# Kernel optimization log

Hardware: AMD Instinct MI355X
Metric: run time of the kernel (lower is better)

The kernel has to match this reference:

```python
import jax, jax.numpy as jnp
import numpy as np

P = 2          # SamplesLoss p=2
BLUR = 0.05    # eps_final = BLUR**P = 0.0025
SCALING = 0.8  # annealing factor per iteration (on the blur scale)


def _cost(x, y):
    # geomloss cost for p=2: |x - y|^2 / 2, shape (N, M)
    x2 = jnp.sum(x * x, axis=-1)
    y2 = jnp.sum(y * y, axis=-1)
    return 0.5 * (x2[:, None] + y2[None, :] - 2.0 * (x @ y.T))


def _softmin(eps, C, h):
    # -eps * log sum_j exp(h_j - C_ij / eps); h already contains log-weights
    return -eps * jax.nn.logsumexp(h[None, :] - C / eps, axis=1)


def _eps_schedule(x, y):
    # geomloss scaling_parameters / epsilon_schedule with diameter from bounding box
    xn, yn = np.asarray(x), np.asarray(y)
    mins = np.minimum(xn.min(0), yn.min(0))
    maxs = np.maximum(xn.max(0), yn.max(0))
    diameter = float(np.linalg.norm(maxs - mins))
    eps_list = ([diameter ** P]
                + [float(np.exp(e)) for e in np.arange(P * np.log(diameter), P * np.log(BLUR), P * np.log(SCALING))]
                + [BLUR ** P])
    return eps_list


def _sinkhorn_divergence(x, y, eps_list):
    # Debiased Sinkhorn divergence S_eps(x, y), geomloss sinkhorn_tensorized
    N, M = x.shape[0], y.shape[0]
    sg = jax.lax.stop_gradient
    C_xy, C_yx = _cost(x, y), _cost(y, x)
    C_xx, C_yy = _cost(x, sg(x)), _cost(y, sg(y))  # geomloss detaches 2nd arg
    # The annealing loop runs with autograd disabled in geomloss:
    Cxy_, Cyx_, Cxx_, Cyy_ = sg(C_xy), sg(C_yx), sg(C_xx), sg(C_yy)
    a_log = jnp.full((N,), -np.log(N), dtype=x.dtype)  # log uniform weights
    b_log = jnp.full((M,), -np.log(M), dtype=y.dtype)
    e0 = eps_list[0]
    f_aa = _softmin(e0, Cxx_, a_log)
    g_bb = _softmin(e0, Cyy_, b_log)
    g_ab = _softmin(e0, Cyx_, a_log)
    f_ba = _softmin(e0, Cxy_, b_log)
    for eps in eps_list:  # fixed schedule, not a data-dim loop
        ft_ba = _softmin(eps, Cxy_, b_log + g_ab / eps)
        gt_ab = _softmin(eps, Cyx_, a_log + f_ba / eps)
        ft_aa = _softmin(eps, Cxx_, a_log + f_aa / eps)
        gt_bb = _softmin(eps, Cyy_, b_log + g_bb / eps)
        f_ba, g_ab = 0.5 * (f_ba + ft_ba), 0.5 * (g_ab + gt_ab)
        f_aa, g_bb = 0.5 * (f_aa + ft_aa), 0.5 * (g_bb + gt_bb)
    # Final extrapolation step (the only one geomloss differentiates through):
    eps = eps_list[-1]
    f_ba, g_ab = (_softmin(eps, C_xy, sg(b_log + g_ab / eps)),
                  _softmin(eps, C_yx, sg(a_log + f_ba / eps)))
    f_aa = _softmin(eps, C_xx, sg(a_log + f_aa / eps))
    g_bb = _softmin(eps, C_yy, sg(b_log + g_bb / eps))
    # scal with uniform weights == mean
    return jnp.mean(f_ba - f_aa) + jnp.mean(g_ab - g_bb)


def setup_inputs() -> dict:
    key = jax.random.key(0)
    kx, kt = jax.random.split(key)
    x = jax.random.normal(kx, (4096, 64), dtype=jnp.float32)
    target = jax.random.normal(kt, (4096, 64), dtype=jnp.float32)
    return {"x": x, "target": target}


def reference(x, target):
    eps_list = _eps_schedule(x, target)  # concrete schedule from data diameter
    return _sinkhorn_divergence(x, target, eps_list)
```

## Files before the change

### kernel.cpp

```cpp
#include <hip/hip_runtime.h>
#include <math.h>

#define NPTS 4096
#define DIM  64
#define MAX_ITERS 37

#define ALOG (-8.317766166719343f)
#define L2E  (1.4426950408889634f)
#define LN2  (0.6931471805599453f)

#define SEA 8388608.0f
#define SEB 1064872507.0f

#if __has_builtin(__builtin_amdgcn_exp2f)
#define EXP2F(x) __builtin_amdgcn_exp2f(x)
#else
#define EXP2F(x) exp2f(x)
#endif
#if __has_builtin(__builtin_amdgcn_logf)
#define LOG2F(x) __builtin_amdgcn_logf(x)
#else
#define LOG2F(x) log2f(x)
#endif

typedef _Float16 f16x8 __attribute__((ext_vector_type(8)));
typedef float    f32x4 __attribute__((ext_vector_type(4)));

__device__ __forceinline__ float aload(const float* p) {
    return __hip_atomic_load(p, __ATOMIC_RELAXED, __HIP_MEMORY_SCOPE_AGENT);
}
__device__ __forceinline__ void astore(float* p, float v) {
    __hip_atomic_store(p, v, __ATOMIC_RELAXED, __HIP_MEMORY_SCOPE_AGENT);
}

template <bool FENCE>
__device__ __forceinline__ void gbar(int* st, int idx, int nsub, int* lsense) {
    __syncthreads();
    if (threadIdx.x == 0) {
        int s = *lsense ^ 1;
        if (FENCE) __threadfence();
        int sub = idx >> 5;
        int prev = __hip_atomic_fetch_add(st + sub * 16, 1, __ATOMIC_ACQ_REL,
                                          __HIP_MEMORY_SCOPE_AGENT);
        if (prev == 31) {
            int pm = __hip_atomic_fetch_add(st + 1536, 1, __ATOMIC_ACQ_REL,
                                            __HIP_MEMORY_SCOPE_AGENT);
            if (pm == nsub - 1) {
                for (int i = 0; i < nsub; i++)
                    __hip_atomic_store(st + i * 16, 0, __ATOMIC_RELAXED,
                                       __HIP_MEMORY_SCOPE_AGENT);
                __hip_atomic_store(st + 1536, 0, __ATOMIC_RELAXED,
                                   __HIP_MEMORY_SCOPE_AGENT);
                __hip_atomic_store(st + 1600, s, __ATOMIC_RELEASE,
                                   __HIP_MEMORY_SCOPE_AGENT);
            } else {
                while (__hip_atomic_load(st + 1600, __ATOMIC_ACQUIRE,
                                         __HIP_MEMORY_SCOPE_AGENT) != s)
                    __builtin_amdgcn_s_sleep(2);
            }
        } else {
            while (__hip_atomic_load(st + 1600, __ATOMIC_ACQUIRE,
                                     __HIP_MEMORY_SCOPE_AGENT) != s)
                __builtin_amdgcn_s_sleep(2);
        }
        *lsense = s;
        if (FENCE) __threadfence();
    }
    __syncthreads();
}

__global__ __launch_bounds__(256, 4) void mega10_kernel(
        const float* __restrict__ x, const float* __restrict__ y,
        _Float16* __restrict__ X16, _Float16* __restrict__ Y16,
        float* __restrict__ x2, float* __restrict__ y2,
        float* __restrict__ pmn, float* __restrict__ pmx,
        int* hdr, float* __restrict__ sched,
        float* H, float* P,
        int* bar, float* __restrict__ out)
{
    const int b  = blockIdx.x;
    const int tt = threadIdx.x;
    int senseA = 0, senseB = 0, senseG = 0;

    const int grp = b >> 9;
    int* barA = bar + grp * 2048;
    int* barB = bar + 4096 + grp * 2048;
    int* barG = bar + 8192;
    const int idxL = b & 511;

    __shared__ float hs[256];
    __shared__ _Float16 Bs[2][64][72];

    {
        int g = b * 256 + tt;
        if (g < NPTS * DIM) {
            float xv = x[g], yv = y[g];
            X16[g] = (_Float16)xv;
            Y16[g] = (_Float16)yv;
            float sx = xv * xv, sy = yv * yv;
            for (int o = 32; o > 0; o >>= 1) {
                sx += __shfl_xor(sx, o, 64);
                sy += __shfl_xor(sy, o, 64);
            }
            if ((tt & 63) == 0) { x2[g >> 6] = sx; y2[g >> 6] = sy; }
        }
        if (b < 128) {
            float mn = INFINITY, mx = -INFINITY;
            for (int gg = b * 256 + tt; gg < NPTS * DIM; gg += 128 * 256) {
                float v = x[gg]; mn = fminf(mn, v); mx = fmaxf(mx, v);
                float w = y[gg]; mn = fminf(mn, w); mx = fmaxf(mx, w);
            }
            float* smn = hs;
            float* smx = (float*)&Bs[0][0][0];
            smn[tt] = mn; smx[tt] = mx;
            __syncthreads();
            if (tt < 64) {
                for (int qq = 1; qq < 4; qq++) {
                    mn = fminf(mn, smn[tt + 64 * qq]);
                    mx = fmaxf(mx, smx[tt + 64 * qq]);
                }
                pmn[b * 64 + tt] = mn;
                pmx[b * 64 + tt] = mx;
            }
        }
    }
    gbar<true>(barG, b, 32, &senseG);

    if (b == 0) {
        float* r2 = hs;
        if (tt < 64) {
            float mn = INFINITY, mx = -INFINITY;
            for (int bb = 0; bb < 128; bb++) {
                mn = fminf(mn, pmn[bb * 64 + tt]);
                mx = fmaxf(mx, pmx[bb * 64 + tt]);
            }
            float range = mx - mn;
            r2[tt] = range * range;
        }
        __syncthreads();
        if (tt == 0) {
            float ss = 0.f;
            for (int k = 0; k < 64; k++) ss += r2[k];
            float diam_f = sqrtf(ss);
            double diam = (double)diam_f;
            double start = 2.0 * log(diam);
            double stop  = 2.0 * log(0.05);
            double step  = 2.0 * log(0.8);
            int n_ar = (int)ceil((stop - start) / step);
            if (n_ar < 0) n_ar = 0;
            int ne = n_ar + 2;
            if (ne > 63) ne = 63;
            sched[0] = (float)(diam * diam);
            for (int k = 0; k < n_ar && (1 + k) < 63; k++)
                sched[1 + k] = (float)exp(start + step * (double)k);
            sched[ne - 1] = 0.0025f;
            for (int k = ne; k < 64; k++) sched[k] = 0.0025f;
            hdr[0] = ne;
        }
    }
    gbar<true>(barG, b, 32, &senseG);

    const int n_eps = *(volatile int*)hdr;

    const int mat = b >> 8, rb = (b >> 4) & 15, cs = b & 15;
    const _Float16* Am = (mat == 0 || mat == 2) ? X16 : Y16;
    const _Float16* Bm = (mat == 1 || mat == 2) ? X16 : Y16;
    const int matc = (mat < 2) ? (1 - mat) : mat;
    const float* sqc = (matc == 0 || matc == 2) ? x2 : y2;
    const int c0 = cs * 256, r0 = rb * 256;
    const int wv = tt >> 6, lane = tt & 63, q = lane >> 4, lo = lane & 15;
    const int srow = tt >> 2, scol = (tt & 3) * 16;

    f16x8 a[4][2];
#pragma unroll
    for (int rt = 0; rt < 4; rt++) {
        const _Float16* ar = Am + (size_t)(r0 + wv * 64 + rt * 16 + lo) * DIM + q * 8;
        a[rt][0] = *(const f16x8*)ar;
        a[rt][1] = *(const f16x8*)(ar + 32);
    }
    const _Float16* Bsrc0 = Bm + (size_t)(c0 + srow) * DIM + scol;

    const bool isComb = (rb < 4) && (tt < 64);
    int   combRow = 0;
    float combSq = 0.f, fprev = 0.f;
    if (rb < 4) {
        combRow = (cs * 4 + rb) * 64 + (tt & 63);
        combSq  = sqc[combRow];
    }

    auto run_main = [&](int t) {
        f16x8 t0a = *(const f16x8*)Bsrc0;
        f16x8 t0b = *(const f16x8*)(Bsrc0 + 8);

        if (t == -2) {
            float inv2i = L2E / sched[0];
            hs[tt] = ALOG * L2E - 0.5f * sqc[c0 + tt] * inv2i;
        } else {
            hs[tt] = aload(&H[mat * 4096 + c0 + tt]);
        }

        int idx = (t == -2) ? 0 : ((t == -1) ? n_eps - 1 : t);
        float inv2 = L2E / sched[idx];

        *(f16x8*)&Bs[0][srow][scol]     = t0a;
        *(f16x8*)&Bs[0][srow][scol + 8] = t0b;

        float m[4] = { -1e30f, -1e30f, -1e30f, -1e30f };
        float s[4] = { 0.f, 0.f, 0.f, 0.f };

        for (int ct = 0; ct < 4; ct++) {
            __syncthreads();
            f16x8 n0, n1;
            if (ct < 3) {
                const _Float16* src = Bsrc0 + (size_t)(ct + 1) * 64 * DIM;
                n0 = *(const f16x8*)src;
                n1 = *(const f16x8*)(src + 8);
            }
            const _Float16 (*Bt)[72] = Bs[ct & 1];
#pragma unroll
            for (int cc = 0; cc < 4; cc++) {
                const _Float16* br = &Bt[cc * 16 + lo][q * 8];
                f16x8 b0 = *(const f16x8*)br;
                f16x8 b1 = *(const f16x8*)(br + 32);
                f32x4 hv = *(const f32x4*)&hs[ct * 64 + cc * 16 + q * 4];
#pragma unroll
                for (int rt = 0; rt < 4; rt++) {
                    f32x4 acc = {0.f, 0.f, 0.f, 0.f};
                    acc = __builtin_amdgcn_mfma_f32_16x16x32_f16(b0, a[rt][0], acc, 0, 0, 0);
                    acc = __builtin_amdgcn_mfma_f32_16x16x32_f16(b1, a[rt][1], acc, 0, 0, 0);
                    float v0 = fmaf(acc[0], inv2, hv[0]);
                    float v1 = fmaf(acc[1], inv2, hv[1]);
                    float v2 = fmaf(acc[2], inv2, hv[2]);
                    float v3 = fmaf(acc[3], inv2, hv[3]);
                    float lm = fmaxf(fmaxf(v0, v1), fmaxf(v2, v3));
                    if (__any(lm > m[rt] + 40.0f)) {
                        float nm = fmaxf(m[rt], lm);
                        s[rt] *= EXP2F(m[rt] - nm);
                        m[rt] = nm;
                    }
                    if (lm > m[rt] - 126.0f) {
                        float mm = m[rt];
                        float e0 = fmaxf(fmaf(v0 - mm, SEA, SEB), 0.f);
                        float e1 = fmaxf(fmaf(v1 - mm, SEA, SEB), 0.f);
                        float e2 = fmaxf(fmaf(v2 - mm, SEA, SEB), 0.f);
                        float e3 = fmaxf(fmaf(v3 - mm, SEA, SEB), 0.f);
                        s[rt] += (__uint_as_float((unsigned)e0)
                                + __uint_as_float((unsigned)e1))
                               + (__uint_as_float((unsigned)e2)
                                + __uint_as_float((unsigned)e3));
                    }
                }
            }
            if (ct < 3) {
                *(f16x8*)&Bs[(ct + 1) & 1][srow][scol]     = n0;
                *(f16x8*)&Bs[(ct + 1) & 1][srow][scol + 8] = n1;
            }
        }

        float ml[4] = { m[0], m[1], m[2], m[3] };
#pragma unroll
        for (int off = 16; off < 64; off <<= 1)
#pragma unroll
            for (int rt = 0; rt < 4; rt++)
                m[rt] = fmaxf(m[rt], __shfl_xor(m[rt], off, 64));
#pragma unroll
        for (int rt = 0; rt < 4; rt++)
            s[rt] *= EXP2F(ml[rt] - m[rt]);
#pragma unroll
        for (int off = 16; off < 64; off <<= 1)
#pragma unroll
            for (int rt = 0; rt < 4; rt++)
                s[rt] += __shfl_xor(s[rt], off, 64);

        if (q == 0) {
            int pw = (t == -1) ? (n_eps & 1) : ((t == -2) ? 1 : (t & 1));
            float* Pw = P + pw * 524288;
            float* Sw = Pw + 262144;
#pragma unroll
            for (int rt = 0; rt < 4; rt++) {
                int row = r0 + wv * 64 + rt * 16 + lo;
                astore(&Pw[(mat * 16 + cs) * NPTS + row], m[rt]);
                astore(&Sw[(mat * 16 + cs) * NPTS + row], s[rt]);
            }
        }
        __syncthreads();
    };

    run_main(-2);
    for (int c = 0; c <= n_eps; c++) {
        gbar<false>(barA, idxL, 16, &senseA);
        if (isComb) {
            int pp = (c == 0) ? 1 : ((c - 1) & 1);
            const float* Pm = P + pp * 524288;
            const float* Ps = Pm + 262144;
            float epsp  = sched[(c == 0) ? 0 : (c - 1)];
            float inv2c = L2E / sched[c];
            int base = (matc * 16) * NPTS + combRow;
            float pv[16], sv[16];
#pragma unroll
            for (int qq = 0; qq < 16; qq++) {
                pv[qq] = aload(&Pm[base + qq * NPTS]);
                sv[qq] = aload(&Ps[base + qq * NPTS]);
            }
            float M = -INFINITY, S = 0.f;
#pragma unroll
            for (int qq = 0; qq < 16; qq++) {
                if (pv[qq] > M) { S *= EXP2F(M - pv[qq]); M = pv[qq]; }
                S += sv[qq] * EXP2F(pv[qq] - M);
            }
            float res  = 0.5f * combSq - epsp * LN2 * (M + LOG2F(S));
            float fnew = (c == 0) ? res : 0.5f * (fprev + res);
            fprev = fnew;
            astore(&H[mat * 4096 + combRow],
                   ALOG * L2E + (fnew - 0.5f * combSq) * inv2c);
        }
        gbar<false>(barB, idxL, 16, &senseB);
        if (c < n_eps) run_main(c);
    }
    run_main(-1);

    gbar<true>(barG, b, 32, &senseG);

    if (b < 64) {
        const float* Pm = P + (n_eps & 1) * 524288;
        const float* Ps = Pm + 262144;
        int g = b * 256 + tt;
        int fmat = g >> 12, row = g & 4095;
        float eps = sched[n_eps - 1];
        const float* sqr = (fmat == 0 || fmat == 2) ? x2 : y2;
        int base = (fmat * 16) * NPTS + row;
        float pv[16], sv[16];
#pragma unroll
        for (int qq = 0; qq < 16; qq++) {
            pv[qq] = aload(&Pm[base + qq * NPTS]);
            sv[qq] = aload(&Ps[base + qq * NPTS]);
        }
        float M = -INFINITY, S = 0.f;
#pragma unroll
        for (int qq = 0; qq < 16; qq++) {
            if (pv[qq] > M) { S *= EXP2F(M - pv[qq]); M = pv[qq]; }
            S += sv[qq] * EXP2F(pv[qq] - M);
        }
        float res = 0.5f * sqr[row] - eps * LN2 * (M + LOG2F(S));
        float val = ((fmat < 2) ? res : -res) * (1.0f / NPTS);
        float* sh = hs;
        sh[tt] = val;
        __syncthreads();
        for (int o = 128; o > 0; o >>= 1) {
            if (tt < o) sh[tt] += sh[tt + o];
            __syncthreads();
        }
        if (tt == 0) atomicAdd(out, sh[0]);
    }
}

__global__ __launch_bounds__(256, 8) void mega9_kernel(
        const float* __restrict__ x, const float* __restrict__ y,
        _Float16* __restrict__ X16, _Float16* __restrict__ Y16,
        float* __restrict__ x2, float* __restrict__ y2,
        float* __restrict__ pmn, float* __restrict__ pmx,
        int* hdr, float* __restrict__ sched,
        float* H, float* P,
        int* bar, float* __restrict__ out)
{
    const int b  = blockIdx.x;
    const int tt = threadIdx.x;
    int senseA = 0, senseB = 0, senseG = 0;

    const int grp = b >> 10;
    int* barA = bar + grp * 2048;
    int* barB = bar + 4096 + grp * 2048;
    int* barG = bar + 8192;
    const int idxL = b & 1023;

    __shared__ float hs[256];
    __shared__ _Float16 Bs[2][64][72];

    {
        int g = b * 256 + tt;
        if (g < NPTS * DIM) {
            float xv = x[g], yv = y[g];
            X16[g] = (_Float16)xv;
            Y16[g] = (_Float16)yv;
            float sx = xv * xv, sy = yv * yv;
            for (int o = 32; o > 0; o >>= 1) {
                sx += __shfl_xor(sx, o, 64);
                sy += __shfl_xor(sy, o, 64);
            }
            if ((tt & 63) == 0) { x2[g >> 6] = sx; y2[g >> 6] = sy; }
        }
        if (b < 128) {
            float mn = INFINITY, mx = -INFINITY;
            for (int gg = b * 256 + tt; gg < NPTS * DIM; gg += 128 * 256) {
                float v = x[gg]; mn = fminf(mn, v); mx = fmaxf(mx, v);
                float w = y[gg]; mn = fminf(mn, w); mx = fmaxf(mx, w);
            }
            float* smn = hs;
            float* smx = (float*)&Bs[0][0][0];
            smn[tt] = mn; smx[tt] = mx;
            __syncthreads();
            if (tt < 64) {
                for (int qq = 1; qq < 4; qq++) {
                    mn = fminf(mn, smn[tt + 64 * qq]);
                    mx = fmaxf(mx, smx[tt + 64 * qq]);
                }
                pmn[b * 64 + tt] = mn;
                pmx[b * 64 + tt] = mx;
            }
        }
    }
    gbar<true>(barG, b, 64, &senseG);

    if (b == 0) {
        float* r2 = hs;
        if (tt < 64) {
            float mn = INFINITY, mx = -INFINITY;
            for (int bb = 0; bb < 128; bb++) {
                mn = fminf(mn, pmn[bb * 64 + tt]);
                mx = fmaxf(mx, pmx[bb * 64 + tt]);
            }
            float range = mx - mn;
            r2[tt] = range * range;
        }
        __syncthreads();
        if (tt == 0) {
            float ss = 0.f;
            for (int k = 0; k < 64; k++) ss += r2[k];
            float diam_f = sqrtf(ss);
            double diam = (double)diam_f;
            double start = 2.0 * log(diam);
            double stop  = 2.0 * log(0.05);
            double step  = 2.0 * log(0.8);
            int n_ar = (int)ceil((stop - start) / step);
            if (n_ar < 0) n_ar = 0;
            int ne = n_ar + 2;
            if (ne > 63) ne = 63;
            sched[0] = (float)(diam * diam);
            for (int k = 0; k < n_ar && (1 + k) < 63; k++)
                sched[1 + k] = (float)exp(start + step * (double)k);
            sched[ne - 1] = 0.0025f;
            for (int k = ne; k < 64; k++) sched[k] = 0.0025f;
            hdr[0] = ne;
        }
    }
    gbar<true>(barG, b, 64, &senseG);

    const int n_eps = *(volatile int*)hdr;

    const int mat = b >> 9, rb = (b >> 4) & 31, cs = b & 15;
    const _Float16* Am = (mat == 0 || mat == 2) ? X16 : Y16;
    const _Float16* Bm = (mat == 1 || mat == 2) ? X16 : Y16;
    const int matc = (mat < 2) ? (1 - mat) : mat;
    const float* sqc = (matc == 0 || matc == 2) ? x2 : y2;
    const int c0 = cs * 256, r0 = rb * 128;
    const int wv = tt >> 6, lane = tt & 63, q = lane >> 4, lo = lane & 15;
    const int srow = tt >> 2, scol = (tt & 3) * 16;

    f16x8 a[2][2];
#pragma unroll
    for (int rt = 0; rt < 2; rt++) {
        const _Float16* ar = Am + (size_t)(r0 + wv * 32 + rt * 16 + lo) * DIM + q * 8;
        a[rt][0] = *(const f16x8*)ar;
        a[rt][1] = *(const f16x8*)(ar + 32);
    }
    const _Float16* Bsrc0 = Bm + (size_t)(c0 + srow) * DIM + scol;

    const bool isComb = (rb < 4) && (tt < 64);
    int   combRow = 0;
    float combSq = 0.f, fprev = 0.f;
    if (rb < 4) {
        combRow = (cs * 4 + rb) * 64 + (tt & 63);
        combSq  = sqc[combRow];
    }

    auto run_main = [&](int t) {
        f16x8 t0a = *(const f16x8*)Bsrc0;
        f16x8 t0b = *(const f16x8*)(Bsrc0 + 8);

        if (t == -2) {
            float inv2i = L2E / sched[0];
            hs[tt] = ALOG * L2E - 0.5f * sqc[c0 + tt] * inv2i;
        } else {
            hs[tt] = aload(&H[mat * 4096 + c0 + tt]);
        }

        int idx = (t == -2) ? 0 : ((t == -1) ? n_eps - 1 : t);
        float inv2 = L2E / sched[idx];

        *(f16x8*)&Bs[0][srow][scol]     = t0a;
        *(f16x8*)&Bs[0][srow][scol + 8] = t0b;

        float m[2] = { -1e30f, -1e30f };
        float s[2] = { 0.f, 0.f };

        for (int ct = 0; ct < 4; ct++) {
            __syncthreads();
            f16x8 n0, n1;
            if (ct < 3) {
                const _Float16* src = Bsrc0 + (size_t)(ct + 1) * 64 * DIM;
                n0 = *(const f16x8*)src;
                n1 = *(const f16x8*)(src + 8);
            }
            const _Float16 (*Bt)[72] = Bs[ct & 1];
#pragma unroll
            for (int cc = 0; cc < 4; cc++) {
                const _Float16* br = &Bt[cc * 16 + lo][q * 8];
                f16x8 b0 = *(const f16x8*)br;
                f16x8 b1 = *(const f16x8*)(br + 32);
                f32x4 hv = *(const f32x4*)&hs[ct * 64 + cc * 16 + q * 4];
#pragma unroll
                for (int rt = 0; rt < 2; rt++) {
                    f32x4 acc = {0.f, 0.f, 0.f, 0.f};
                    acc = __builtin_amdgcn_mfma_f32_16x16x32_f16(b0, a[rt][0], acc, 0, 0, 0);
                    acc = __builtin_amdgcn_mfma_f32_16x16x32_f16(b1, a[rt][1], acc, 0, 0, 0);
                    float v0 = fmaf(acc[0], inv2, hv[0]);
                    float v1 = fmaf(acc[1], inv2, hv[1]);
                    float v2 = fmaf(acc[2], inv2, hv[2]);
                    float v3 = fmaf(acc[3], inv2, hv[3]);
                    float lm = fmaxf(fmaxf(v0, v1), fmaxf(v2, v3));
                    if (__any(lm > m[rt] + 40.0f)) {
                        float nm = fmaxf(m[rt], lm);
                        s[rt] *= EXP2F(m[rt] - nm);
                        m[rt] = nm;
                    }
                    if (lm > m[rt] - 126.0f) {
                        float mm = m[rt];
                        float e0 = fmaxf(fmaf(v0 - mm, SEA, SEB), 0.f);
                        float e1 = fmaxf(fmaf(v1 - mm, SEA, SEB), 0.f);
                        float e2 = fmaxf(fmaf(v2 - mm, SEA, SEB), 0.f);
                        float e3 = fmaxf(fmaf(v3 - mm, SEA, SEB), 0.f);
                        s[rt] += (__uint_as_float((unsigned)e0)
                                + __uint_as_float((unsigned)e1))
                               + (__uint_as_float((unsigned)e2)
                                + __uint_as_float((unsigned)e3));
                    }
                }
            }
            if (ct < 3) {
                *(f16x8*)&Bs[(ct + 1) & 1][srow][scol]     = n0;
                *(f16x8*)&Bs[(ct + 1) & 1][srow][scol + 8] = n1;
            }
        }

        float ml[2] = { m[0], m[1] };
#pragma unroll
        for (int off = 16; off < 64; off <<= 1)
#pragma unroll
            for (int rt = 0; rt < 2; rt++)
                m[rt] = fmaxf(m[rt], __shfl_xor(m[rt], off, 64));
#pragma unroll
        for (int rt = 0; rt < 2; rt++)
            s[rt] *= EXP2F(ml[rt] - m[rt]);
#pragma unroll
        for (int off = 16; off < 64; off <<= 1)
#pragma unroll
            for (int rt = 0; rt < 2; rt++)
                s[rt] += __shfl_xor(s[rt], off, 64);

        if (q == 0) {
            int pw = (t == -1) ? (n_eps & 1) : ((t == -2) ? 1 : (t & 1));
            float* Pw = P + pw * 524288;
            float* Sw = Pw + 262144;
#pragma unroll
            for (int rt = 0; rt < 2; rt++) {
                int row = r0 + wv * 32 + rt * 16 + lo;
                astore(&Pw[(mat * 16 + cs) * NPTS + row], m[rt]);
                astore(&Sw[(mat * 16 + cs) * NPTS + row], s[rt]);
            }
        }
        __syncthreads();
    };

    run_main(-2);
    for (int c = 0; c <= n_eps; c++) {
        gbar<false>(barA, idxL, 32, &senseA);
        if (isComb) {
            int pp = (c == 0) ? 1 : ((c - 1) & 1);
            const float* Pm = P + pp * 524288;
            const float* Ps = Pm + 262144;
            float epsp  = sched[(c == 0) ? 0 : (c - 1)];
            float inv2c = L2E / sched[c];
            int base = (matc * 16) * NPTS + combRow;
            float M = -INFINITY, S = 0.f;
#pragma unroll
            for (int qq = 0; qq < 16; qq++) {
                float pv = aload(&Pm[base + qq * NPTS]);
                float sv = aload(&Ps[base + qq * NPTS]);
                if (pv > M) { S *= EXP2F(M - pv); M = pv; }
                S += sv * EXP2F(pv - M);
            }
            float res  = 0.5f * combSq - epsp * LN2 * (M + LOG2F(S));
            float fnew = (c == 0) ? res : 0.5f * (fprev + res);
            fprev = fnew;
            astore(&H[mat * 4096 + combRow],
                   ALOG * L2E + (fnew - 0.5f * combSq) * inv2c);
        }
        gbar<false>(barB, idxL, 32, &senseB);
        if (c < n_eps) run_main(c);
    }
    run_main(-1);

    gbar<true>(barG, b, 64, &senseG);

    if (b < 64) {
        const float* Pm = P + (n_eps & 1) * 524288;
        const float* Ps = Pm + 262144;
        int g = b * 256 + tt;
        int fmat = g >> 12, row = g & 4095;
        float eps = sched[n_eps - 1];
        const float* sqr = (fmat == 0 || fmat == 2) ? x2 : y2;
        int base = (fmat * 16) * NPTS + row;
        float M = -INFINITY, S = 0.f;
#pragma unroll
        for (int qq = 0; qq < 16; qq++) {
            float pv = aload(&Pm[base + qq * NPTS]);
            float sv = aload(&Ps[base + qq * NPTS]);
            if (pv > M) { S *= EXP2F(M - pv); M = pv; }
            S += sv * EXP2F(pv - M);
        }
        float res = 0.5f * sqr[row] - eps * LN2 * (M + LOG2F(S));
        float val = ((fmat < 2) ? res : -res) * (1.0f / NPTS);
        float* sh = hs;
        sh[tt] = val;
        __syncthreads();
        for (int o = 128; o > 0; o >>= 1) {
            if (tt < o) sh[tt] += sh[tt + o];
            __syncthreads();
        }
        if (tt == 0) atomicAdd(out, sh[0]);
    }
}

__global__ void minmax_part_kernel(const float* __restrict__ x,
                                   const float* __restrict__ y,
                                   float* __restrict__ partmn,
                                   float* __restrict__ partmx) {
    int t = threadIdx.x;
    int bid = blockIdx.x;
    int g0 = bid * 256 + t;
    const int total = NPTS * DIM;
    float mn = INFINITY, mx = -INFINITY;
    for (int g = g0; g < total; g += 128 * 256) {
        float v = x[g]; mn = fminf(mn, v); mx = fmaxf(mx, v);
        float w = y[g]; mn = fminf(mn, w); mx = fmaxf(mx, w);
    }
    __shared__ float smn[256], smx[256];
    smn[t] = mn; smx[t] = mx;
    __syncthreads();
    if (t < 64) {
        for (int q = 1; q < 4; q++) {
            mn = fminf(mn, smn[t + 64 * q]);
            mx = fmaxf(mx, smx[t + 64 * q]);
        }
        partmn[bid * 64 + t] = mn;
        partmx[bid * 64 + t] = mx;
    }
}

__global__ void schedule_kernel(const float* __restrict__ partmn,
                                const float* __restrict__ partmx,
                                int* __restrict__ hdr,
                                float* __restrict__ sched) {
    int d = threadIdx.x;
    float mn = INFINITY, mx = -INFINITY;
    for (int b = 0; b < 128; b++) {
        mn = fminf(mn, partmn[b * 64 + d]);
        mx = fmaxf(mx, partmx[b * 64 + d]);
    }
    float range = mx - mn;
    __shared__ float r2[64];
    r2[d] = range * range;
    __syncthreads();
    if (d == 0) {
        float ss = 0.f;
        for (int k = 0; k < 64; k++) ss += r2[k];
        float diam_f = sqrtf(ss);
        double diam = (double)diam_f;
        double start = 2.0 * log(diam);
        double stop  = 2.0 * log(0.05);
        double step  = 2.0 * log(0.8);
        int n_eps = (int)ceil((stop - start) / step);
        if (n_eps < 0) n_eps = 0;
        n_eps += 2;
        if (n_eps > 63) n_eps = 63;
        sched[0] = (float)(diam * diam);
        for (int k = 0; k < n_eps - 2 && (1 + k) < 63; k++)
            sched[1 + k] = (float)exp(start + step * (double)k);
        sched[n_eps - 1] = 0.0025f;
        for (int k = n_eps; k < 64; k++) sched[k] = 0.0025f;
        hdr[0] = n_eps;
    }
}

__global__ void sqnorm_kernel(const float* __restrict__ X, float* __restrict__ out) {
    int wave = (blockIdx.x * blockDim.x + threadIdx.x) >> 6;
    int lane = threadIdx.x & 63;
    if (wave >= NPTS) return;
    float v = X[wave * DIM + lane];
    float s = v * v;
    for (int o = 32; o > 0; o >>= 1) s += __shfl_xor(s, o, 64);
    if (lane == 0) out[wave] = s;
}

__global__ void cast_kernel(const float* __restrict__ x, const float* __restrict__ y,
                            _Float16* __restrict__ X16, _Float16* __restrict__ Y16) {
    int g = blockIdx.x * 256 + threadIdx.x;
    X16[g] = (_Float16)x[g];
    Y16[g] = (_Float16)y[g];
}

__global__ __launch_bounds__(256, 4) void pass_kernel(
        const _Float16* __restrict__ X16, const _Float16* __restrict__ Y16,
        const float* __restrict__ x2, const float* __restrict__ y2,
        float* __restrict__ F, float* __restrict__ H, float* __restrict__ P,
        const int* __restrict__ hdr, const float* __restrict__ sched, int t) {
    const int n_eps = hdr[0];
    if (t >= 0 && t > n_eps) return;

    int b = blockIdx.x;
    int mat = b >> 8, rb = (b >> 3) & 31, cs = b & 7;
    const _Float16* Am = (mat == 0 || mat == 2) ? X16 : Y16;
    const _Float16* Bm = (mat == 1 || mat == 2) ? X16 : Y16;
    int matc = (mat < 2) ? (1 - mat) : mat;
    const float* sqc = (matc == 0 || matc == 2) ? x2 : y2;

    __shared__ float hs[512];
    __shared__ _Float16 Bs[2][64][72];

    int tt = threadIdx.x;
    int c0 = cs * 512, r0 = rb * 128;

    if (t == -2) {
        float inv2i = L2E / sched[0];
        for (int r = tt; r < 512; r += 256)
            hs[r] = ALOG * L2E - 0.5f * sqc[c0 + r] * inv2i;
    } else if (t == -1) {
        for (int r = tt; r < 512; r += 256)
            hs[r] = H[mat * 4096 + c0 + r];
    } else {
        int pp = (t == 0) ? 1 : ((t - 1) & 1);
        const float* Pm = P + pp * 262144;
        const float* Ps = Pm + 131072;
        float epsp = sched[(t == 0) ? 0 : (t - 1)];
        float inv2c = L2E / sched[t];
        for (int r = tt; r < 512; r += 256) {
            int row = c0 + r;
            int base = (matc * 8) * NPTS + row;
            float M = -INFINITY;
#pragma unroll
            for (int q = 0; q < 8; q++) M = fmaxf(M, Pm[base + q * NPTS]);
            float S = 0.f;
#pragma unroll
            for (int q = 0; q < 8; q++)
                S += Ps[base + q * NPTS] * EXP2F(Pm[base + q * NPTS] - M);
            float sq = sqc[row];
            float res = 0.5f * sq - epsp * LN2 * (M + LOG2F(S));
            float fnew = (t == 0) ? res
                       : 0.5f * (F[((t - 1) & 1) * 16384 + matc * 4096 + row] + res);
            float h = ALOG * L2E + (fnew - 0.5f * sq) * inv2c;
            hs[r] = h;
            if (rb == 0) {
                F[(t & 1) * 16384 + matc * 4096 + row] = fnew;
                H[mat * 4096 + row] = h;
            }
        }
    }
    __syncthreads();
    if (t >= 0 && t >= n_eps) return;

    int idx = (t == -2) ? 0 : ((t == -1) ? n_eps - 1 : t);
    float inv2 = L2E / sched[idx];

    int wv = tt >> 6, lane = tt & 63, q = lane >> 4, lo = lane & 15;

    f16x8 a[2][2];
#pragma unroll
    for (int rt = 0; rt < 2; rt++) {
        const _Float16* ar = Am + (size_t)(r0 + wv * 32 + rt * 16 + lo) * DIM + q * 8;
        a[rt][0] = *(const f16x8*)ar;
        a[rt][1] = *(const f16x8*)(ar + 32);
    }

    int srow = tt >> 2, scol = (tt & 3) * 16;
    {
        const _Float16* src = Bm + (size_t)(c0 + srow) * DIM + scol;
        *(f16x8*)&Bs[0][srow][scol]     = *(const f16x8*)src;
        *(f16x8*)&Bs[0][srow][scol + 8] = *(const f16x8*)(src + 8);
    }

    float m[2][4], s[2][4];
#pragma unroll
    for (int rt = 0; rt < 2; rt++)
#pragma unroll
        for (int r = 0; r < 4; r++) { m[rt][r] = -INFINITY; s[rt][r] = 0.f; }

    for (int ct = 0; ct < 8; ct++) {
        __syncthreads();
        f16x8 n0, n1;
        if (ct < 7) {
            const _Float16* src = Bm + (size_t)(c0 + (ct + 1) * 64 + srow) * DIM + scol;
            n0 = *(const f16x8*)src;
            n1 = *(const f16x8*)(src + 8);
        }
        const _Float16 (*Bt)[72] = Bs[ct & 1];
        float v[2][4][4];
#pragma unroll
        for (int cc = 0; cc < 4; cc++) {
            const _Float16* br = &Bt[cc * 16 + lo][q * 8];
            f16x8 b0 = *(const f16x8*)br;
            f16x8 b1 = *(const f16x8*)(br + 32);
            float hval = hs[ct * 64 + cc * 16 + lo];
#pragma unroll
            for (int rt = 0; rt < 2; rt++) {
                f32x4 acc = {0.f, 0.f, 0.f, 0.f};
                acc = __builtin_amdgcn_mfma_f32_16x16x32_f16(a[rt][0], b0, acc, 0, 0, 0);
                acc = __builtin_amdgcn_mfma_f32_16x16x32_f16(a[rt][1], b1, acc, 0, 0, 0);
#pragma unroll
                for (int r = 0; r < 4; r++) v[rt][r][cc] = fmaf(acc[r], inv2, hval);
            }
        }
#pragma unroll
        for (int rt = 0; rt < 2; rt++)
#pragma unroll
            for (int r = 0; r < 4; r++) {
                float lm = fmaxf(fmaxf(v[rt][r][0], v[rt][r][1]),
                                 fmaxf(v[rt][r][2], v[rt][r][3]));
                if (lm > m[rt][r] - 26.0f) {
                    float nm = fmaxf(m[rt][r], lm);
                    float acc = s[rt][r] * EXP2F(m[rt][r] - nm);
                    acc += EXP2F(v[rt][r][0] - nm) + EXP2F(v[rt][r][1] - nm)
                         + EXP2F(v[rt][r][2] - nm) + EXP2F(v[rt][r][3] - nm);
                    m[rt][r] = nm; s[rt][r] = acc;
                }
            }
        if (ct < 7) {
            *(f16x8*)&Bs[(ct + 1) & 1][srow][scol]     = n0;
            *(f16x8*)&Bs[(ct + 1) & 1][srow][scol + 8] = n1;
        }
    }

#pragma unroll
    for (int off = 1; off < 16; off <<= 1) {
#pragma unroll
        for (int rt = 0; rt < 2; rt++)
#pragma unroll
            for (int r = 0; r < 4; r++) {
                float om = __shfl_xor(m[rt][r], off, 64);
                float os = __shfl_xor(s[rt][r], off, 64);
                float nm = fmaxf(m[rt][r], om);
                s[rt][r] = s[rt][r] * EXP2F(m[rt][r] - nm) + os * EXP2F(om - nm);
                m[rt][r] = nm;
            }
    }
    if (lo == 0) {
        int pw = (t == -1) ? (n_eps & 1) : ((t == -2) ? 1 : (t & 1));
        float* Pm = P + pw * 262144;
        float* Ps = Pm + 131072;
#pragma unroll
        for (int rt = 0; rt < 2; rt++)
#pragma unroll
            for (int r = 0; r < 4; r++) {
                int row = r0 + wv * 32 + rt * 16 + q * 4 + r;
                Pm[(mat * 8 + cs) * NPTS + row] = m[rt][r];
                Ps[(mat * 8 + cs) * NPTS + row] = s[rt][r];
            }
    }
}

__global__ void finalize_kernel(const float* __restrict__ P,
                                const float* __restrict__ x2, const float* __restrict__ y2,
                                const int* __restrict__ hdr, const float* __restrict__ sched,
                                float* __restrict__ out) {
    int n_eps = hdr[0];
    const float* Pm = P + (n_eps & 1) * 262144;
    const float* Ps = Pm + 131072;
    int g = blockIdx.x * 256 + threadIdx.x;
    int mat = g >> 12, row = g & 4095;
    float eps = sched[n_eps - 1];
    const float* sqr = (mat == 0 || mat == 2) ? x2 : y2;
    int base = (mat * 8) * NPTS + row;
    float M = -INFINITY;
#pragma unroll
    for (int q = 0; q < 8; q++) M = fmaxf(M, Pm[base + q * NPTS]);
    float S = 0.f;
#pragma unroll
    for (int q = 0; q < 8; q++) S += Ps[base + q * NPTS] * EXP2F(Pm[base + q * NPTS] - M);
    float res = 0.5f * sqr[row] - eps * LN2 * (M + LOG2F(S));
    float val = ((mat == 0 || mat == 1) ? res : -res) * (1.0f / NPTS);
    __shared__ float sh[256];
    sh[threadIdx.x] = val;
    __syncthreads();
    for (int o = 128; o > 0; o >>= 1) {
        if (threadIdx.x < o) sh[threadIdx.x] += sh[threadIdx.x + o];
        __syncthreads();
    }
    if (threadIdx.x == 0) atomicAdd(out, sh[0]);
}

extern "C" void kernel_launch(void* const* d_in, const int* in_sizes, int n_in,
                              void* d_out, int out_size, void* d_ws, size_t ws_size,
                              hipStream_t stream) {
    const float* x = (const float*)d_in[0];
    const float* y = (const float*)d_in[1];
    float* out = (float*)d_out;
    float* w = (float*)d_ws;

    int*   hdr   = (int*)w;
    float* sched = w + 16;
    float* pmn   = w + 80;
    float* pmx   = w + 8272;
    float* x2    = w + 16464;
    float* y2    = w + 20560;
    float* F     = w + 24656;
    float* H     = w + 57424;
    float* P     = w + 73808;

    _Float16* X16c = (_Float16*)(w + 598096);
    _Float16* Y16c = (_Float16*)(w + 729168);

    _Float16* X16e = (_Float16*)(w + 1122384);
    _Float16* Y16e = (_Float16*)(w + 1253456);
    int*      bare = (int*)(w + 1384528);
    const size_t ws_need_e = (size_t)(1384528 + 10240 + 16) * 4;

    hipMemsetAsync(out, 0, sizeof(float), stream);

    int occ10 = 0, occ9 = 0;
    (void)hipOccupancyMaxActiveBlocksPerMultiprocessor(&occ10, mega10_kernel, 256, 0);
    (void)hipOccupancyMaxActiveBlocksPerMultiprocessor(&occ9, mega9_kernel, 256, 0);

    if (occ10 >= 4 && ws_size >= ws_need_e) {
        hipMemsetAsync(bare, 0, 5 * 2048 * sizeof(int), stream);
        hipLaunchKernelGGL(mega10_kernel, dim3(1024), dim3(256), 0, stream,
                           x, y, X16e, Y16e, x2, y2, pmn, pmx, hdr, sched,
                           H, P, bare, out);
    } else if (occ9 >= 8 && ws_size >= ws_need_e) {
        hipMemsetAsync(bare, 0, 5 * 2048 * sizeof(int), stream);
        hipLaunchKernelGGL(mega9_kernel, dim3(2048), dim3(256), 0, stream,
                           x, y, X16e, Y16e, x2, y2, pmn, pmx, hdr, sched,
                           H, P, bare, out);
    } else {
        hipLaunchKernelGGL(minmax_part_kernel, dim3(128), dim3(256), 0, stream, x, y, pmn, pmx);
        hipLaunchKernelGGL(schedule_kernel, dim3(1), dim3(64), 0, stream, pmn, pmx, hdr, sched);
        hipLaunchKernelGGL(sqnorm_kernel, dim3(1024), dim3(256), 0, stream, x, x2);
        hipLaunchKernelGGL(sqnorm_kernel, dim3(1024), dim3(256), 0, stream, y, y2);
        hipLaunchKernelGGL(cast_kernel, dim3(1024), dim3(256), 0, stream, x, y, X16c, Y16c);
        hipLaunchKernelGGL(pass_kernel, dim3(1024), dim3(256), 0, stream,
                           X16c, Y16c, x2, y2, F, H, P, hdr, sched, -2);
        for (int t = 0; t < MAX_ITERS; t++)
            hipLaunchKernelGGL(pass_kernel, dim3(1024), dim3(256), 0, stream,
                               X16c, Y16c, x2, y2, F, H, P, hdr, sched, t);
        hipLaunchKernelGGL(pass_kernel, dim3(1024), dim3(256), 0, stream,
                           X16c, Y16c, x2, y2, F, H, P, hdr, sched, -1);
        hipLaunchKernelGGL(finalize_kernel, dim3(64), dim3(256), 0, stream,
                           P, x2, y2, hdr, sched, out);
    }
}
```

Baseline: 956.9 us.

## Replace per-iteration grid barriers with fine-grained producer/consumer flags

The two group-wide barriers per annealing iteration are replaced by per-block release/acquire flags. Each combine block waits only on the 16 partial-logsumexp producers for its rows, and each main block waits only on the 4 combine blocks that write its H slice. H is double-buffered (H0/H1), so a fast block can move on to the next iteration while slower blocks still read the old potentials. This is meant to cut barrier latency and straggler stalls, at the cost of more flag traffic, spin-polling, and subtle ordering risks around the P double buffer.

```diff
diff --git a/kernel.cpp b/kernel.cpp
--- a/kernel.cpp
+++ b/kernel.cpp
@@ -31,6 +31,12 @@
 }
 __device__ __forceinline__ void astore(float* p, float v) {
     __hip_atomic_store(p, v, __ATOMIC_RELAXED, __HIP_MEMORY_SCOPE_AGENT);
+}
+__device__ __forceinline__ int aload_acq(const int* p) {
+    return __hip_atomic_load(p, __ATOMIC_ACQUIRE, __HIP_MEMORY_SCOPE_AGENT);
+}
+__device__ __forceinline__ void astore_rel(int* p, int v) {
+    __hip_atomic_store(p, v, __ATOMIC_RELEASE, __HIP_MEMORY_SCOPE_AGENT);
 }
 
 template <bool FENCE>
@@ -69,24 +75,19 @@
     __syncthreads();
 }
 
-__global__ __launch_bounds__(256, 4) void mega10_kernel(
+__global__ __launch_bounds__(256, 4) void mega11_kernel(
         const float* __restrict__ x, const float* __restrict__ y,
         _Float16* __restrict__ X16, _Float16* __restrict__ Y16,
         float* __restrict__ x2, float* __restrict__ y2,
         float* __restrict__ pmn, float* __restrict__ pmx,
         int* hdr, float* __restrict__ sched,
-        float* H, float* P,
-        int* bar, float* __restrict__ out)
+        float* H0, float* H1, float* P,
+        int* bar, int* flagP, int* flagH, float* __restrict__ out)
 {
     const int b  = blockIdx.x;
     const int tt = threadIdx.x;
-    int senseA = 0, senseB = 0, senseG = 0;
-
-    const int grp = b >> 9;
-    int* barA = bar + grp * 2048;
-    int* barB = bar + 4096 + grp * 2048;
+    int senseG = 0;
     int* barG = bar + 8192;
-    const int idxL = b & 511;
 
     __shared__ float hs[256];
     __shared__ _Float16 Bs[2][64][72];
@@ -180,15 +181,20 @@
     }
     const _Float16* Bsrc0 = Bm + (size_t)(c0 + srow) * DIM + scol;
 
-    const bool isComb = (rb < 4) && (tt < 64);
+    const bool combRole = (rb < 4);
     int   combRow = 0;
     float combSq = 0.f, fprev = 0.f;
-    if (rb < 4) {
+    if (combRole) {
         combRow = (cs * 4 + rb) * 64 + (tt & 63);
         combSq  = sqc[combRow];
     }
 
-    auto run_main = [&](int t) {
+    int*       flagPown = flagP + ((mat * 16 + rb) * 16 + cs) * 16;
+    const int* flagPsrc = flagP + ((matc * 16 + cs) * 16 + (tt & 15)) * 16;
+    int*       flagHown = flagH + (mat * 64 + cs * 4 + rb) * 16;
+    const int* flagHsrc = flagH + (mat * 64 + cs * 4 + (lane & 3)) * 16;
+
+    auto run_main = [&](int t, const float* Hp) {
         f16x8 t0a = *(const f16x8*)Bsrc0;
         f16x8 t0b = *(const f16x8*)(Bsrc0 + 8);
 
@@ -196,7 +202,7 @@
             float inv2i = L2E / sched[0];
             hs[tt] = ALOG * L2E - 0.5f * sqc[c0 + tt] * inv2i;
         } else {
-            hs[tt] = aload(&H[mat * 4096 + c0 + tt]);
+            hs[tt] = aload(&Hp[mat * 4096 + c0 + tt]);
         }
 
         int idx = (t == -2) ? 0 : ((t == -1) ? n_eps - 1 : t);
@@ -284,40 +290,59 @@
             }
         }
         __syncthreads();
+        if (tt == 0)
+            astore_rel(flagPown,
+                       (t == -2) ? 1 : ((t == -1) ? n_eps + 2 : t + 2));
     };
 
-    run_main(-2);
+    run_main(-2, (const float*)0);
     for (int c = 0; c <= n_eps; c++) {
-        gbar<false>(barA, idxL, 16, &senseA);
-        if (isComb) {
-            int pp = (c == 0) ? 1 : ((c - 1) & 1);
-            const float* Pm = P + pp * 524288;
-            const float* Ps = Pm + 262144;
-            float epsp  = sched[(c == 0) ? 0 : (c - 1)];
-            float inv2c = L2E / sched[c];
-            int base = (matc * 16) * NPTS + combRow;
-            float pv[16], sv[16];
-#pragma unroll
-            for (int qq = 0; qq < 16; qq++) {
-                pv[qq] = aload(&Pm[base + qq * NPTS]);
-                sv[qq] = aload(&Ps[base + qq * NPTS]);
-            }
-            float M = -INFINITY, S = 0.f;
-#pragma unroll
-            for (int qq = 0; qq < 16; qq++) {
-                if (pv[qq] > M) { S *= EXP2F(M - pv[qq]); M = pv[qq]; }
-                S += sv[qq] * EXP2F(pv[qq] - M);
-            }
-            float res  = 0.5f * combSq - epsp * LN2 * (M + LOG2F(S));
-            float fnew = (c == 0) ? res : 0.5f * (fprev + res);
-            fprev = fnew;
-            astore(&H[mat * 4096 + combRow],
-                   ALOG * L2E + (fnew - 0.5f * combSq) * inv2c);
-        }
-        gbar<false>(barB, idxL, 16, &senseB);
-        if (c < n_eps) run_main(c);
-    }
-    run_main(-1);
+        if (combRole) {
+            if (tt < 64) {
+                const int tgt = c + 1;
+                while (!__all(aload_acq(flagPsrc) >= tgt))
+                    __builtin_amdgcn_s_sleep(1);
+                int pp = (c == 0) ? 1 : ((c - 1) & 1);
+                const float* Pm = P + pp * 524288;
+                const float* Ps = Pm + 262144;
+                float epsp  = sched[(c == 0) ? 0 : (c - 1)];
+                float inv2c = L2E / sched[c];
+                int base = (matc * 16) * NPTS + combRow;
+                float pv[16], sv[16];
+#pragma unroll
+                for (int qq = 0; qq < 16; qq++) {
+                    pv[qq] = aload(&Pm[base + qq * NPTS]);
+                    sv[qq] = aload(&Ps[base + qq * NPTS]);
+                }
+                float M = -INFINITY, S = 0.f;
+#pragma unroll
+                for (int qq = 0; qq < 16; qq++) {
+                    if (pv[qq] > M) { S *= EXP2F(M - pv[qq]); M = pv[qq]; }
+                    S += sv[qq] * EXP2F(pv[qq] - M);
+                }
+                float res  = 0.5f * combSq - epsp * LN2 * (M + LOG2F(S));
+                float fnew = (c == 0) ? res : 0.5f * (fprev + res);
+                fprev = fnew;
+                float* Hc = (c & 1) ? H1 : H0;
+                astore(&Hc[mat * 4096 + combRow],
+                       ALOG * L2E + (fnew - 0.5f * combSq) * inv2c);
+            }
+            __syncthreads();
+            if (tt == 0) astore_rel(flagHown, c + 1);
+        }
+        if (c < n_eps) {
+            const int tgt = c + 1;
+            while (!__all(aload_acq(flagHsrc) >= tgt))
+                __builtin_amdgcn_s_sleep(1);
+            run_main(c, (c & 1) ? H1 : H0);
+        }
+    }
+    {
+        const int tgt = n_eps + 1;
+        while (!__all(aload_acq(flagHsrc) >= tgt))
+            __builtin_amdgcn_s_sleep(1);
+        run_main(-1, (n_eps & 1) ? H1 : H0);
+    }
 
     gbar<true>(barG, b, 32, &senseG);
 
@@ -921,20 +946,24 @@
     _Float16* X16e = (_Float16*)(w + 1122384);
     _Float16* Y16e = (_Float16*)(w + 1253456);
     int*      bare = (int*)(w + 1384528);
-    const size_t ws_need_e = (size_t)(1384528 + 10240 + 16) * 4;
+    int*      flagP = (int*)(w + 1394768);
+    int*      flagH = (int*)(w + 1411152);
+    const size_t ws_need_9  = (size_t)(1384528 + 10240 + 16) * 4;
+    const size_t ws_need_11 = (size_t)(1411152 + 4096 + 16) * 4;
 
     hipMemsetAsync(out, 0, sizeof(float), stream);
 
-    int occ10 = 0, occ9 = 0;
-    (void)hipOccupancyMaxActiveBlocksPerMultiprocessor(&occ10, mega10_kernel, 256, 0);
+    int occ11 = 0, occ9 = 0;
+    (void)hipOccupancyMaxActiveBlocksPerMultiprocessor(&occ11, mega11_kernel, 256, 0);
     (void)hipOccupancyMaxActiveBlocksPerMultiprocessor(&occ9, mega9_kernel, 256, 0);
 
-    if (occ10 >= 4 && ws_size >= ws_need_e) {
+    if (occ11 >= 4 && ws_size >= ws_need_11) {
         hipMemsetAsync(bare, 0, 5 * 2048 * sizeof(int), stream);
-        hipLaunchKernelGGL(mega10_kernel, dim3(1024), dim3(256), 0, stream,
+        hipMemsetAsync(flagP, 0, (16384 + 4096) * sizeof(int), stream);
+        hipLaunchKernelGGL(mega11_kernel, dim3(1024), dim3(256), 0, stream,
                            x, y, X16e, Y16e, x2, y2, pmn, pmx, hdr, sched,
-                           H, P, bare, out);
-    } else if (occ9 >= 8 && ws_size >= ws_need_e) {
+                           H, F, P, bare, flagP, flagH, out);
+    } else if (occ9 >= 8 && ws_size >= ws_need_9) {
         hipMemsetAsync(bare, 0, 5 * 2048 * sizeof(int), stream);
         hipLaunchKernelGGL(mega9_kernel, dim3(2048), dim3(256), 0, stream,
                            x, y, X16e, Y16e, x2, y2, pmn, pmx, hdr, sched,
```

Result: slower. 978.4 us (+2.2%).
